# Kernel tuning notes

Measured on AMD Instinct MI355X. Metric: run time of the kernel, lower is better.

## Reference

```python
import jax, jax.numpy as jnp
import numpy as np

NUM_HEADS = 16
D_KV = 64
NUM_BUCKETS = 32
MAX_DISTANCE = 128
LN_EPS = 1e-6


def _relative_position_bucket(seq_len):
    # bidirectional T5 bucketing
    ctx = jnp.arange(seq_len)[:, None]
    mem = jnp.arange(seq_len)[None, :]
    rel = mem - ctx  # [S, S]
    nb = NUM_BUCKETS // 2
    buckets = (rel > 0).astype(jnp.int32) * nb
    rel_abs = jnp.abs(rel)
    max_exact = nb // 2
    is_small = rel_abs < max_exact
    large = max_exact + (
        jnp.log(jnp.maximum(rel_abs, 1).astype(jnp.float32) / max_exact)
        / np.log(MAX_DISTANCE / max_exact)
        * (nb - max_exact)
    ).astype(jnp.int32)
    large = jnp.minimum(large, nb - 1)
    buckets = buckets + jnp.where(is_small, rel_abs, large)
    return buckets  # [S, S] int32


def setup_inputs() -> dict:
    key = jax.random.key(0)
    ks = jax.random.split(key, 6)
    B, S, D = 2, 2048, 1024
    scale = 1.0 / np.sqrt(D)
    return {
        "hidden_states": jax.random.normal(ks[0], (B, S, D), jnp.float32),
        "ln_weight": jnp.ones((D,), jnp.float32),
        "wq": jax.random.normal(ks[1], (D, NUM_HEADS * D_KV), jnp.float32) * scale,
        "wk": jax.random.normal(ks[2], (D, NUM_HEADS * D_KV), jnp.float32) * scale,
        "wv": jax.random.normal(ks[3], (D, NUM_HEADS * D_KV), jnp.float32) * scale,
        "wo": jax.random.normal(ks[4], (NUM_HEADS * D_KV, D), jnp.float32) * scale,
        "rel_bias": jax.random.normal(ks[5], (NUM_BUCKETS, NUM_HEADS), jnp.float32) * 0.1,
    }


def reference(hidden_states, ln_weight, wq, wk, wv, wo, rel_bias):
    B, S, D = hidden_states.shape
    # T5LayerNorm: RMS norm (no mean subtraction, no bias)
    var = jnp.mean(jnp.square(hidden_states), axis=-1, keepdims=True)
    normed = hidden_states * jax.lax.rsqrt(var + LN_EPS) * ln_weight

    def proj(w):
        return (normed @ w).reshape(B, S, NUM_HEADS, D_KV).transpose(0, 2, 1, 3)

    q = proj(wq)  # [B, H, S, dk]
    k = proj(wk)
    v = proj(wv)

    # T5 does NOT scale by sqrt(d_kv)
    scores = jnp.einsum("bhqd,bhkd->bhqk", q, k)

    buckets = _relative_position_bucket(S)           # [S, S]
    pos_bias = rel_bias[buckets]                     # [S, S, H]
    pos_bias = pos_bias.transpose(2, 0, 1)[None]     # [1, H, S, S]
    scores = scores + pos_bias

    attn = jax.nn.softmax(scores, axis=-1)
    ctx = jnp.einsum("bhqk,bhkd->bhqd", attn, v)
    ctx = ctx.transpose(0, 2, 1, 3).reshape(B, S, NUM_HEADS * D_KV)
    attn_out = ctx @ wo

    # dropout in eval mode -> identity; residual add
    return hidden_states + attn_out
```

## Files before the change

### kernel.cpp

```cpp
#include <hip/hip_runtime.h>

using s4     = __attribute__((ext_vector_type(4))) short;
using s8     = __attribute__((ext_vector_type(8))) short;
using f32x4  = __attribute__((ext_vector_type(4))) float;
using f32x4u = __attribute__((ext_vector_type(4), aligned(4))) float;

__device__ __forceinline__ float bf2f(short u) {
    union { unsigned int i; float f; } c;
    c.i = ((unsigned int)(unsigned short)u) << 16;
    return c.f;
}
__device__ __forceinline__ short f2bf(float f) {
    union { float f; unsigned int i; } c; c.f = f;
    unsigned int x = c.i;
    x += 0x7fffu + ((x >> 16) & 1u);
    return (short)(x >> 16);
}
__device__ __forceinline__ unsigned int cvt_pk_bf16(float lo, float hi) {
    unsigned int r;
    asm("v_cvt_pk_bf16_f32 %0, %1, %2" : "=v"(r) : "v"(lo), "v"(hi));
    return r;
}
__device__ __forceinline__ void gload16(const short* g, const char* lds) {
    __builtin_amdgcn_global_load_lds(
        (const __attribute__((address_space(1))) unsigned int*)(unsigned long long)(const void*)g,
        (__attribute__((address_space(3))) unsigned int*)(unsigned int)(unsigned long long)(const void*)lds,
        16, 0, 0);
}

#define MFMA(a, b, c) __builtin_amdgcn_mfma_f32_16x16x32_bf16(a, b, c, 0, 0, 0)
#define LOG2E 1.4426950408889634f

__global__ __launch_bounds__(256) void convT_kernel(const float* __restrict__ in,
                                                    short* __restrict__ out) {
    __shared__ float t[64][65];
    int n0 = blockIdx.x * 64, k0 = blockIdx.y * 64;
    int tx = threadIdx.x & 15, ty = threadIdx.x >> 4;
#pragma unroll
    for (int i = 0; i < 4; ++i) {
        int r = ty + i * 16;
        f32x4 v = *(const f32x4*)(in + (size_t)(k0 + r) * 1024 + n0 + tx * 4);
        t[r][tx * 4 + 0] = v[0]; t[r][tx * 4 + 1] = v[1];
        t[r][tx * 4 + 2] = v[2]; t[r][tx * 4 + 3] = v[3];
    }
    __syncthreads();
#pragma unroll
    for (int i = 0; i < 4; ++i) {
        int r = ty + i * 16;
        s4 o;
#pragma unroll
        for (int e = 0; e < 4; ++e) o[e] = f2bf(t[tx * 4 + e][r]);
        *(s4*)(out + (size_t)(n0 + r) * 1024 + k0 + tx * 4) = o;
    }
}

__global__ __launch_bounds__(256) void rmsnorm_kernel(const float* __restrict__ x,
                                                      const float* __restrict__ w,
                                                      short* __restrict__ out) {
    int row = blockIdx.x;
    int tid = threadIdx.x;
    const float* xr = x + ((size_t)row << 10);
    f32x4 v = *(const f32x4*)(xr + tid * 4);
    float ss = v[0] * v[0] + v[1] * v[1] + v[2] * v[2] + v[3] * v[3];
#pragma unroll
    for (int off = 32; off > 0; off >>= 1) ss += __shfl_down(ss, off);
    __shared__ float red[4];
    if ((tid & 63) == 0) red[tid >> 6] = ss;
    __syncthreads();
    float total = red[0] + red[1] + red[2] + red[3];
    float r = rsqrtf(total * (1.0f / 1024.0f) + 1e-6f);
    f32x4 wv = *(const f32x4*)(w + tid * 4);
    s4 o;
    o[0] = f2bf(v[0] * r * wv[0]);
    o[1] = f2bf(v[1] * r * wv[1]);
    o[2] = f2bf(v[2] * r * wv[2]);
    o[3] = f2bf(v[3] * r * wv[3]);
    *(s4*)(out + ((size_t)row << 10) + tid * 4) = o;
}

__global__ void bias_table_kernel(const float* __restrict__ rel_bias, float* __restrict__ table) {
    int idx = blockIdx.x * 256 + threadIdx.x;
    if (idx >= 4095) return;
    int rel = 2047 - idx;
    int bucket = (rel > 0) ? 16 : 0;
    int a = (rel < 0) ? -rel : rel;
    if (a < 8) {
        bucket += a;
    } else {
        float l = logf((float)a * 0.125f) / 2.772588722239781f * 8.0f;
        int large = 8 + (int)l;
        bucket += (large > 15) ? 15 : large;
    }
#pragma unroll
    for (int h = 0; h < 16; ++h)
        table[h * 4095 + idx] = rel_bias[bucket * 16 + h] * LOG2E;
}

template<int BN, int WROWS, int WCOLS, int MODE>
__global__ __launch_bounds__(256) void gemm2(const short* __restrict__ A,
                                             const short* __restrict__ Bt,
                                             short* __restrict__ oq,
                                             short* __restrict__ ok,
                                             short* __restrict__ ov,
                                             float* __restrict__ Cf,
                                             const float* __restrict__ resid) {
    constexpr int MI = 128 / WROWS / 16;
    constexpr int NI = BN / WCOLS / 16;
    constexpr int NA = 4;
    constexpr int NB = BN / 32;
    const int K = 1024;
    __shared__ __align__(16) char lds[(128 + BN) * 128];
    char* A_base = lds;
    char* B_base = lds + 128 * 128;

    int tid = threadIdx.x;
    int m0 = blockIdx.y << 7, n0 = blockIdx.x * BN;
    int w = tid >> 6, l = tid & 63;
    int lr = l & 15, lg = l >> 4;
    int wm = (w / WCOLS) * (128 / WROWS);
    int wn = (w % WCOLS) * (BN / WCOLS);
    int sr = l >> 3;
    int cs = (l & 7) ^ sr;

    f32x4 acc[MI][NI] = {};

    for (int kk = 0; kk < K; kk += 64) {
        __syncthreads();
#pragma unroll
        for (int i = 0; i < NA; ++i) {
            int r = (w * NA + i) * 8 + sr;
            gload16(A + (size_t)(m0 + r) * K + kk + cs * 8, A_base + (w * NA + i) * 1024);
        }
#pragma unroll
        for (int i = 0; i < NB; ++i) {
            int r = (w * NB + i) * 8 + sr;
            gload16(Bt + (size_t)(n0 + r) * K + kk + cs * 8, B_base + (w * NB + i) * 1024);
        }
        __syncthreads();

        s8 af[2][MI], bfv[2][NI];
#pragma unroll
        for (int ks = 0; ks < 2; ++ks) {
            int chunk = ((ks * 4 + lg) ^ (lr & 7)) << 4;
#pragma unroll
            for (int mi = 0; mi < MI; ++mi)
                af[ks][mi] = *(const s8*)(A_base + (wm + mi * 16 + lr) * 128 + chunk);
#pragma unroll
            for (int ni = 0; ni < NI; ++ni)
                bfv[ks][ni] = *(const s8*)(B_base + (wn + ni * 16 + lr) * 128 + chunk);
        }
#pragma unroll
        for (int ks = 0; ks < 2; ++ks)
#pragma unroll
            for (int mi = 0; mi < MI; ++mi)
#pragma unroll
                for (int ni = 0; ni < NI; ++ni)
                    acc[mi][ni] = MFMA(af[ks][mi], bfv[ks][ni], acc[mi][ni]);
    }

#pragma unroll
    for (int mi = 0; mi < MI; ++mi) {
#pragma unroll
        for (int ni = 0; ni < NI; ++ni) {
#pragma unroll
            for (int j = 0; j < 4; ++j) {
                int r = m0 + wm + mi * 16 + lg * 4 + j;
                int c = n0 + wn + ni * 16 + lr;
                float v = acc[mi][ni][j];
                if (MODE == 0) {
                    size_t idx = ((size_t)r << 10) + c;
                    Cf[idx] = v + resid[idx];
                } else {
                    int b = r >> 11, sdx = r & 2047;
                    int which = c >> 10, nn = c & 1023;
                    int h = nn >> 6, d = nn & 63;
                    if (which == 0)
                        oq[(((size_t)(b * 16 + h) << 11) + sdx) * 64 + d] = f2bf(v * LOG2E);
                    else if (which == 1)
                        ok[(((size_t)(b * 16 + h) << 11) + sdx) * 64 + d] = f2bf(v);
                    else
                        ov[((size_t)((b * 16 + h) * 64 + d) << 11) + sdx] = f2bf(v);
                }
            }
        }
    }
}

__global__ __launch_bounds__(256) void attn_kernel(const short* __restrict__ Q,
                                                   const short* __restrict__ Km,
                                                   const short* __restrict__ VT,
                                                   const float* __restrict__ tabR,
                                                   short* __restrict__ ctx) {
    const int S = 2048;
    int bid = blockIdx.x;
    int qt = bid >> 5;
    int bh = ((bid & 7) << 2) | ((bid >> 3) & 3);
    int b = bh >> 4, h = bh & 15;
    const short* Qp = Q  + (size_t)bh * S * 64;
    const short* Kp = Km + (size_t)bh * S * 64;
    const short* Vp = VT + (size_t)bh * 64 * S;
    const float* tb0 = tabR + h * 4095;

    __shared__ __align__(16) short K_lds[64][72];
    __shared__ __align__(16) short V_lds[64 * 64];
    __shared__ __align__(16) short P_lds[4][16][72];

    int tid = threadIdx.x;
    int wave = tid >> 6, lane = tid & 63;
    int lr = lane & 15, lg = lane >> 4;
    int q0 = qt * 64 + wave * 16;

    const short* qrow = Qp + (size_t)(q0 + lr) * 64 + lg * 8;
    s8 qf0 = *(const s8*)(qrow);
    s8 qf1 = *(const s8*)(qrow + 32);

    f32x4 o_acc[4] = {};
    float m_run = -1e30f, l_run = 0.0f;

    int k_row = tid >> 2, k_c = (tid & 3) << 4;
    int v_d = tid >> 2, v_kc = (tid & 3) << 4;
    int kb0 = v_kc >> 3;
    int v_wr0 = v_d * 128 + ((kb0 ^ (v_d & 7)) << 4);
    int v_wr1 = v_d * 128 + (((kb0 + 1) ^ (v_d & 7)) << 4);

    const short* kp = Kp + (size_t)k_row * 64 + k_c;
    s8 kv0 = *(const s8*)kp, kv1 = *(const s8*)(kp + 8);
    const short* vp = Vp + (size_t)v_d * S + v_kc;
    s8 vv0 = *(const s8*)vp, vv1 = *(const s8*)(vp + 8);

    char* pbase = (char*)P_lds + wave * 2304 + lr * 144;

    for (int kt0 = 0; kt0 < S; kt0 += 64) {
        __syncthreads();
        *(s8*)&K_lds[k_row][k_c] = kv0;
        *(s8*)&K_lds[k_row][k_c + 8] = kv1;
        *(s8*)((char*)V_lds + v_wr0) = vv0;
        *(s8*)((char*)V_lds + v_wr1) = vv1;
        int nt = (kt0 + 64 < S) ? kt0 + 64 : kt0;
        kv0 = *(const s8*)(kp + (size_t)nt * 64);
        kv1 = *(const s8*)(kp + (size_t)nt * 64 + 8);
        vv0 = *(const s8*)(vp + nt);
        vv1 = *(const s8*)(vp + nt + 8);
        __syncthreads();

        const float* tb = tb0 + (q0 + lr - kt0 - lg * 4 + 2044);
        f32x4 sc[4];
        __builtin_amdgcn_s_setprio(1);
#pragma unroll
        for (int kt = 0; kt < 4; ++kt) {
            s8 kf0 = *(const s8*)&K_lds[kt * 16 + lr][lg * 8];
            s8 kf1 = *(const s8*)&K_lds[kt * 16 + lr][32 + lg * 8];
            f32x4 s = {};
            s = MFMA(kf0, qf0, s);
            s = MFMA(kf1, qf1, s);
            sc[kt] = s;
        }
        __builtin_amdgcn_s_setprio(0);
#pragma unroll
        for (int kt = 0; kt < 4; ++kt) {
            f32x4u bv = *(const f32x4u*)(tb - kt * 16);
#pragma unroll
            for (int j = 0; j < 4; ++j) sc[kt][j] += bv[3 - j];
        }

        float mt = sc[0][0];
#pragma unroll
        for (int kt = 0; kt < 4; ++kt)
#pragma unroll
            for (int j = 0; j < 4; ++j) mt = fmaxf(mt, sc[kt][j]);
        mt = fmaxf(mt, __shfl_xor(mt, 16));
        mt = fmaxf(mt, __shfl_xor(mt, 32));

        if (__any(mt > m_run + 11.0f)) {
            float mn = fmaxf(m_run, mt);
            float scale = exp2f(m_run - mn);
            m_run = mn;
            l_run *= scale;
#pragma unroll
            for (int dt = 0; dt < 4; ++dt)
#pragma unroll
                for (int j = 0; j < 4; ++j) o_acc[dt][j] *= scale;
        }

#pragma unroll
        for (int kt = 0; kt < 4; ++kt) {
#pragma unroll
            for (int j = 0; j < 4; ++j) {
                float p = exp2f(sc[kt][j] - m_run);
                sc[kt][j] = p;
                l_run += p;
            }
            uint2 pv;
            pv.x = cvt_pk_bf16(sc[kt][0], sc[kt][1]);
            pv.y = cvt_pk_bf16(sc[kt][2], sc[kt][3]);
            *(uint2*)(pbase + kt * 32 + lg * 8) = pv;
        }

        s8 pf0 = *(const s8*)(pbase + lg * 16);
        s8 pf1 = *(const s8*)(pbase + 64 + lg * 16);
        __builtin_amdgcn_s_setprio(1);
#pragma unroll
        for (int dt = 0; dt < 4; ++dt) {
            int d = dt * 16 + lr;
            s8 vf0 = *(const s8*)((char*)V_lds + d * 128 + ((lg ^ (lr & 7)) << 4));
            s8 vf1 = *(const s8*)((char*)V_lds + d * 128 + (((4 + lg) ^ (lr & 7)) << 4));
            o_acc[dt] = MFMA(vf0, pf0, o_acc[dt]);
            o_acc[dt] = MFMA(vf1, pf1, o_acc[dt]);
        }
        __builtin_amdgcn_s_setprio(0);
    }

    l_run += __shfl_xor(l_run, 16);
    l_run += __shfl_xor(l_run, 32);
    float rl = 1.0f / l_run;

    short* cbase = ctx + ((size_t)(b * 2048 + q0 + lr) << 10) + h * 64 + lg * 4;
#pragma unroll
    for (int dt = 0; dt < 4; ++dt) {
        s4 o;
#pragma unroll
        for (int j = 0; j < 4; ++j) o[j] = f2bf(o_acc[dt][j] * rl);
        *(s4*)(cbase + dt * 16) = o;
    }
}

extern "C" void kernel_launch(void* const* d_in, const int* in_sizes, int n_in,
                              void* d_out, int out_size, void* d_ws, size_t ws_size,
                              hipStream_t stream) {
    const float* hidden = (const float*)d_in[0];
    const float* ln_w   = (const float*)d_in[1];
    const float* wq     = (const float*)d_in[2];
    const float* wk     = (const float*)d_in[3];
    const float* wv     = (const float*)d_in[4];
    const float* wo     = (const float*)d_in[5];
    const float* relb   = (const float*)d_in[6];
    float* out = (float*)d_out;

    char* ws = (char*)d_ws;
    const size_t SZ  = 8388608;
    const size_t WSZ = 2097152;
    short* normed = (short*)(ws);
    short* q      = (short*)(ws + SZ);
    short* k      = (short*)(ws + 2 * SZ);
    short* vt     = (short*)(ws + 3 * SZ);
    short* ctx    = (short*)(ws + 4 * SZ);
    short* wqkv_t = (short*)(ws + 5 * SZ);
    short* wo_t   = (short*)(ws + 5 * SZ + 3 * WSZ);
    float* table  = (float*)(ws + 5 * SZ + 4 * WSZ);

    dim3 tg(16, 16);
    convT_kernel<<<tg, 256, 0, stream>>>(wq, wqkv_t);
    convT_kernel<<<tg, 256, 0, stream>>>(wk, wqkv_t + 1024 * 1024);
    convT_kernel<<<tg, 256, 0, stream>>>(wv, wqkv_t + 2 * 1024 * 1024);
    convT_kernel<<<tg, 256, 0, stream>>>(wo, wo_t);
    rmsnorm_kernel<<<4096, 256, 0, stream>>>(hidden, ln_w, normed);
    bias_table_kernel<<<16, 256, 0, stream>>>(relb, table);
    gemm2<128, 2, 2, 1><<<dim3(24, 32), 256, 0, stream>>>(normed, wqkv_t, q, k, vt, nullptr, nullptr);
    attn_kernel<<<1024, 256, 0, stream>>>(q, k, vt, table, ctx);
    gemm2<64, 4, 1, 0><<<dim3(16, 32), 256, 0, stream>>>(ctx, wo_t, nullptr, nullptr, nullptr, out, hidden);
}
```

Before: 244.7 us.

## Fuse weight transposes, remap GEMM tiles, and streamline attention softmax bookkeeping

Merges the four weight conversion launches into one 3D-grid launch and remaps GEMM workgroup IDs so neighbouring blocks are grouped across the eight XCDs. In attention it swizzles K and P in LDS instead of padding them, seeds the QK MFMA accumulator with the position bias, and computes the row sum with an MFMA against a ones vector instead of scalar adds and shuffles. Together these cut launch overhead and VALU work in the inner loop. The tradeoff is an extra MFMA per tile, and the row sum now comes from bf16-rounded probabilities.

```diff
diff --git a/kernel.cpp b/kernel.cpp
--- a/kernel.cpp
+++ b/kernel.cpp
@@ -31,9 +31,16 @@
 #define MFMA(a, b, c) __builtin_amdgcn_mfma_f32_16x16x32_bf16(a, b, c, 0, 0, 0)
 #define LOG2E 1.4426950408889634f
 
-__global__ __launch_bounds__(256) void convT_kernel(const float* __restrict__ in,
-                                                    short* __restrict__ out) {
+__global__ __launch_bounds__(256) void convT4_kernel(const float* __restrict__ w0,
+                                                     const float* __restrict__ w1,
+                                                     const float* __restrict__ w2,
+                                                     const float* __restrict__ w3,
+                                                     short* __restrict__ oqkv,
+                                                     short* __restrict__ owo) {
     __shared__ float t[64][65];
+    int z = blockIdx.z;
+    const float* in = (z == 0) ? w0 : (z == 1) ? w1 : (z == 2) ? w2 : w3;
+    short* out = (z < 3) ? (oqkv + (size_t)z * 1048576) : owo;
     int n0 = blockIdx.x * 64, k0 = blockIdx.y * 64;
     int tx = threadIdx.x & 15, ty = threadIdx.x >> 4;
 #pragma unroll
@@ -113,8 +120,13 @@
     char* A_base = lds;
     char* B_base = lds + 128 * 128;
 
+    int nbx = gridDim.x;
+    int nwg = nbx * gridDim.y;
+    int lid = blockIdx.y * nbx + blockIdx.x;
+    int nid = (lid & 7) * (nwg >> 3) + (lid >> 3);
+    int m0 = (nid / nbx) << 7, n0 = (nid % nbx) * BN;
+
     int tid = threadIdx.x;
-    int m0 = blockIdx.y << 7, n0 = blockIdx.x * BN;
     int w = tid >> 6, l = tid & 63;
     int lr = l & 15, lg = l >> 4;
     int wm = (w / WCOLS) * (128 / WROWS);
@@ -201,9 +213,9 @@
     const short* Vp = VT + (size_t)bh * 64 * S;
     const float* tb0 = tabR + h * 4095;
 
-    __shared__ __align__(16) short K_lds[64][72];
+    __shared__ __align__(16) short K_lds[64 * 64];
     __shared__ __align__(16) short V_lds[64 * 64];
-    __shared__ __align__(16) short P_lds[4][16][72];
+    __shared__ __align__(16) short P_lds[4][16 * 64];
 
     int tid = threadIdx.x;
     int wave = tid >> 6, lane = tid & 63;
@@ -214,28 +226,40 @@
     s8 qf0 = *(const s8*)(qrow);
     s8 qf1 = *(const s8*)(qrow + 32);
 
+    s8 ones;
+#pragma unroll
+    for (int e = 0; e < 8; ++e) ones[e] = (short)0x3F80;
+
     f32x4 o_acc[4] = {};
-    float m_run = -1e30f, l_run = 0.0f;
-
-    int k_row = tid >> 2, k_c = (tid & 3) << 4;
-    int v_d = tid >> 2, v_kc = (tid & 3) << 4;
-    int kb0 = v_kc >> 3;
-    int v_wr0 = v_d * 128 + ((kb0 ^ (v_d & 7)) << 4);
-    int v_wr1 = v_d * 128 + (((kb0 + 1) ^ (v_d & 7)) << 4);
-
-    const short* kp = Kp + (size_t)k_row * 64 + k_c;
+    f32x4 o_l = {};
+    float m_run = -1e30f;
+
+    int k_row = tid >> 2;
+    int kc0 = (tid & 3) * 2;
+    char* k_wr0 = (char*)K_lds + k_row * 128 + ((kc0 ^ (k_row & 7)) << 4);
+    char* k_wr1 = (char*)K_lds + k_row * 128 + (((kc0 + 1) ^ (k_row & 7)) << 4);
+    char* v_wr0 = (char*)V_lds + k_row * 128 + ((kc0 ^ (k_row & 7)) << 4);
+    char* v_wr1 = (char*)V_lds + k_row * 128 + (((kc0 + 1) ^ (k_row & 7)) << 4);
+
+    const short* kp = Kp + (size_t)k_row * 64 + (tid & 3) * 16;
     s8 kv0 = *(const s8*)kp, kv1 = *(const s8*)(kp + 8);
-    const short* vp = Vp + (size_t)v_d * S + v_kc;
+    const short* vp = Vp + (size_t)k_row * S + (tid & 3) * 16;
     s8 vv0 = *(const s8*)vp, vv1 = *(const s8*)(vp + 8);
 
-    char* pbase = (char*)P_lds + wave * 2304 + lr * 144;
+    char* pbase = (char*)P_lds + wave * 2048 + lr * 128;
+    int psw = lr & 7;
+    const float* tbl = tb0 + (q0 + lr - lg * 4 + 2044);
+
+    const char* kr_base = (const char*)K_lds + lr * 128;
+    int kch0 = (lg ^ (lr & 7)) << 4;
+    int kch1 = ((4 + lg) ^ (lr & 7)) << 4;
 
     for (int kt0 = 0; kt0 < S; kt0 += 64) {
         __syncthreads();
-        *(s8*)&K_lds[k_row][k_c] = kv0;
-        *(s8*)&K_lds[k_row][k_c + 8] = kv1;
-        *(s8*)((char*)V_lds + v_wr0) = vv0;
-        *(s8*)((char*)V_lds + v_wr1) = vv1;
+        *(s8*)k_wr0 = kv0;
+        *(s8*)k_wr1 = kv1;
+        *(s8*)v_wr0 = vv0;
+        *(s8*)v_wr1 = vv1;
         int nt = (kt0 + 64 < S) ? kt0 + 64 : kt0;
         kv0 = *(const s8*)(kp + (size_t)nt * 64);
         kv1 = *(const s8*)(kp + (size_t)nt * 64 + 8);
@@ -243,31 +267,23 @@
         vv1 = *(const s8*)(vp + nt + 8);
         __syncthreads();
 
-        const float* tb = tb0 + (q0 + lr - kt0 - lg * 4 + 2044);
         f32x4 sc[4];
-        __builtin_amdgcn_s_setprio(1);
 #pragma unroll
         for (int kt = 0; kt < 4; ++kt) {
-            s8 kf0 = *(const s8*)&K_lds[kt * 16 + lr][lg * 8];
-            s8 kf1 = *(const s8*)&K_lds[kt * 16 + lr][32 + lg * 8];
-            f32x4 s = {};
+            f32x4u bv = *(const f32x4u*)(tbl - kt0 - kt * 16);
+            f32x4 s = { bv[3], bv[2], bv[1], bv[0] };
+            s8 kf0 = *(const s8*)(kr_base + kt * 2048 + kch0);
+            s8 kf1 = *(const s8*)(kr_base + kt * 2048 + kch1);
             s = MFMA(kf0, qf0, s);
             s = MFMA(kf1, qf1, s);
             sc[kt] = s;
         }
-        __builtin_amdgcn_s_setprio(0);
-#pragma unroll
-        for (int kt = 0; kt < 4; ++kt) {
-            f32x4u bv = *(const f32x4u*)(tb - kt * 16);
-#pragma unroll
-            for (int j = 0; j < 4; ++j) sc[kt][j] += bv[3 - j];
-        }
-
-        float mt = sc[0][0];
-#pragma unroll
-        for (int kt = 0; kt < 4; ++kt)
-#pragma unroll
-            for (int j = 0; j < 4; ++j) mt = fmaxf(mt, sc[kt][j]);
+
+        float m0a = fmaxf(fmaxf(sc[0][0], sc[0][1]), fmaxf(sc[0][2], sc[0][3]));
+        float m1a = fmaxf(fmaxf(sc[1][0], sc[1][1]), fmaxf(sc[1][2], sc[1][3]));
+        float m2a = fmaxf(fmaxf(sc[2][0], sc[2][1]), fmaxf(sc[2][2], sc[2][3]));
+        float m3a = fmaxf(fmaxf(sc[3][0], sc[3][1]), fmaxf(sc[3][2], sc[3][3]));
+        float mt = fmaxf(fmaxf(m0a, m1a), fmaxf(m2a, m3a));
         mt = fmaxf(mt, __shfl_xor(mt, 16));
         mt = fmaxf(mt, __shfl_xor(mt, 32));
 
@@ -275,7 +291,8 @@
             float mn = fmaxf(m_run, mt);
             float scale = exp2f(m_run - mn);
             m_run = mn;
-            l_run *= scale;
+#pragma unroll
+            for (int j = 0; j < 4; ++j) o_l[j] *= scale;
 #pragma unroll
             for (int dt = 0; dt < 4; ++dt)
 #pragma unroll
@@ -285,42 +302,40 @@
 #pragma unroll
         for (int kt = 0; kt < 4; ++kt) {
 #pragma unroll
-            for (int j = 0; j < 4; ++j) {
-                float p = exp2f(sc[kt][j] - m_run);
-                sc[kt][j] = p;
-                l_run += p;
-            }
+            for (int j = 0; j < 4; ++j) sc[kt][j] = exp2f(sc[kt][j] - m_run);
             uint2 pv;
             pv.x = cvt_pk_bf16(sc[kt][0], sc[kt][1]);
             pv.y = cvt_pk_bf16(sc[kt][2], sc[kt][3]);
-            *(uint2*)(pbase + kt * 32 + lg * 8) = pv;
-        }
-
-        s8 pf0 = *(const s8*)(pbase + lg * 16);
-        s8 pf1 = *(const s8*)(pbase + 64 + lg * 16);
+            int sw = ((kt * 2 + (lg >> 1)) ^ psw) << 4;
+            *(uint2*)(pbase + sw + (lg & 1) * 8) = pv;
+        }
+
+        s8 pf0 = *(const s8*)(pbase + ((lg ^ psw) << 4));
+        s8 pf1 = *(const s8*)(pbase + (((4 + lg) ^ psw) << 4));
+        o_l = MFMA(ones, pf0, o_l);
+        o_l = MFMA(ones, pf1, o_l);
         __builtin_amdgcn_s_setprio(1);
 #pragma unroll
         for (int dt = 0; dt < 4; ++dt) {
             int d = dt * 16 + lr;
-            s8 vf0 = *(const s8*)((char*)V_lds + d * 128 + ((lg ^ (lr & 7)) << 4));
-            s8 vf1 = *(const s8*)((char*)V_lds + d * 128 + (((4 + lg) ^ (lr & 7)) << 4));
+            const char* vb = (const char*)V_lds + d * 128;
+            s8 vf0 = *(const s8*)(vb + ((lg ^ (lr & 7)) << 4));
+            s8 vf1 = *(const s8*)(vb + (((4 + lg) ^ (lr & 7)) << 4));
             o_acc[dt] = MFMA(vf0, pf0, o_acc[dt]);
             o_acc[dt] = MFMA(vf1, pf1, o_acc[dt]);
         }
         __builtin_amdgcn_s_setprio(0);
     }
 
-    l_run += __shfl_xor(l_run, 16);
-    l_run += __shfl_xor(l_run, 32);
-    float rl = 1.0f / l_run;
+    float rl = 1.0f / o_l[0];
 
     short* cbase = ctx + ((size_t)(b * 2048 + q0 + lr) << 10) + h * 64 + lg * 4;
 #pragma unroll
     for (int dt = 0; dt < 4; ++dt) {
-        s4 o;
-#pragma unroll
-        for (int j = 0; j < 4; ++j) o[j] = f2bf(o_acc[dt][j] * rl);
-        *(s4*)(cbase + dt * 16) = o;
+        uint2 o;
+        o.x = cvt_pk_bf16(o_acc[dt][0] * rl, o_acc[dt][1] * rl);
+        o.y = cvt_pk_bf16(o_acc[dt][2] * rl, o_acc[dt][3] * rl);
+        *(uint2*)(cbase + dt * 16) = o;
     }
 }
 
@@ -348,11 +363,7 @@
     short* wo_t   = (short*)(ws + 5 * SZ + 3 * WSZ);
     float* table  = (float*)(ws + 5 * SZ + 4 * WSZ);
 
-    dim3 tg(16, 16);
-    convT_kernel<<<tg, 256, 0, stream>>>(wq, wqkv_t);
-    convT_kernel<<<tg, 256, 0, stream>>>(wk, wqkv_t + 1024 * 1024);
-    convT_kernel<<<tg, 256, 0, stream>>>(wv, wqkv_t + 2 * 1024 * 1024);
-    convT_kernel<<<tg, 256, 0, stream>>>(wo, wo_t);
+    convT4_kernel<<<dim3(16, 16, 4), 256, 0, stream>>>(wq, wk, wv, wo, wqkv_t, wo_t);
     rmsnorm_kernel<<<4096, 256, 0, stream>>>(hidden, ln_w, normed);
     bias_table_kernel<<<16, 256, 0, stream>>>(relb, table);
     gemm2<128, 2, 2, 1><<<dim3(24, 32), 256, 0, stream>>>(normed, wqkv_t, q, k, vt, nullptr, nullptr);
```

Measured after the change: 246.1 us. Within noise of the previous version (+0.6%).
